# Kernel tuning notes

Measured on AMD Instinct MI355X. Metric: run time of the kernel, lower is better.

Reference implementation:

```python
import jax, jax.numpy as jnp
import numpy as np

INPUT_DIM, HIDDEN, OUT_DIM = 7, 64, 4


def _lstm_layer(x_seq, W_ih, W_hh, b_ih, b_hh):
    """Single LSTM layer, batch_first x_seq [B,T,D] -> [B,T,H]. PyTorch gate order i,f,g,o."""
    B = x_seq.shape[0]
    H = W_hh.shape[1]
    # Precompute input projection for all timesteps (hoist GEMM out of the scan).
    x_proj = jnp.einsum('btd,gd->btg', x_seq, W_ih) + b_ih + b_hh  # [B,T,4H]

    def step(carry, xt):
        h, c = carry
        gates = xt + h @ W_hh.T  # [B,4H]
        i, f, g, o = jnp.split(gates, 4, axis=-1)
        i = jax.nn.sigmoid(i)
        f = jax.nn.sigmoid(f)
        g = jnp.tanh(g)
        o = jax.nn.sigmoid(o)
        c = f * c + i * g
        h = o * jnp.tanh(c)
        return (h, c), h

    h0 = jnp.zeros((B, H), x_seq.dtype)
    c0 = jnp.zeros((B, H), x_seq.dtype)
    (_, _), hs = jax.lax.scan(step, (h0, c0), jnp.swapaxes(x_proj, 0, 1))  # hs [T,B,H]
    return jnp.swapaxes(hs, 0, 1)  # [B,T,H]


def setup_inputs() -> dict:
    key = jax.random.key(0)
    ks = jax.random.split(key, 12)
    s = 0.1  # init scale ~ 1/sqrt(hidden)
    x = jax.random.normal(ks[0], (4096, 512, INPUT_DIM), dtype=jnp.float32)
    W_ih0 = jax.random.normal(ks[1], (4 * HIDDEN, INPUT_DIM), dtype=jnp.float32) * s
    W_hh0 = jax.random.normal(ks[2], (4 * HIDDEN, HIDDEN), dtype=jnp.float32) * s
    b_ih0 = jax.random.normal(ks[3], (4 * HIDDEN,), dtype=jnp.float32) * s
    b_hh0 = jax.random.normal(ks[4], (4 * HIDDEN,), dtype=jnp.float32) * s
    W_ih1 = jax.random.normal(ks[5], (4 * HIDDEN, HIDDEN), dtype=jnp.float32) * s
    W_hh1 = jax.random.normal(ks[6], (4 * HIDDEN, HIDDEN), dtype=jnp.float32) * s
    b_ih1 = jax.random.normal(ks[7], (4 * HIDDEN,), dtype=jnp.float32) * s
    b_hh1 = jax.random.normal(ks[8], (4 * HIDDEN,), dtype=jnp.float32) * s
    W_fc = jax.random.normal(ks[9], (OUT_DIM, HIDDEN), dtype=jnp.float32) * s
    b_fc = jax.random.normal(ks[10], (OUT_DIM,), dtype=jnp.float32) * s
    return {"x": x, "W_ih0": W_ih0, "W_hh0": W_hh0, "b_ih0": b_ih0, "b_hh0": b_hh0,
            "W_ih1": W_ih1, "W_hh1": W_hh1, "b_ih1": b_ih1, "b_hh1": b_hh1,
            "W_fc": W_fc, "b_fc": b_fc}


def reference(x, W_ih0, W_hh0, b_ih0, b_hh0, W_ih1, W_hh1, b_ih1, b_hh1, W_fc, b_fc):
    h1 = _lstm_layer(x, W_ih0, W_hh0, b_ih0, b_hh0)   # [B,T,H]
    h2 = _lstm_layer(h1, W_ih1, W_hh1, b_ih1, b_hh1)  # [B,T,H]
    last = h2[:, -1, :]                               # [B,H]
    return last @ W_fc.T + b_fc                       # [B,4]
```

## Files before the change

kernel.cpp:

```cpp
#include <hip/hip_runtime.h>

#define T_SEQ 512
#define HID 64
#define MB 16
#define NTHREADS 1024
#define A1STR 104
#define A2STR 72

typedef __attribute__((ext_vector_type(8))) short short8;
typedef __attribute__((ext_vector_type(4))) float floatx4;

#define LOG2E 1.4426950408889634f

__device__ __forceinline__ float bf2f(short b) {
  return __uint_as_float(((unsigned)(unsigned short)b) << 16);
}
__device__ __forceinline__ short f2bf_rne(float v) {
  unsigned u = __float_as_uint(v);
  return (short)((u + 0x7FFFu + ((u >> 16) & 1u)) >> 16);
}
__device__ __forceinline__ float rcp_(float x) { return __builtin_amdgcn_rcpf(x); }
__device__ __forceinline__ float sigm_p(float ap) {
  return rcp_(1.f + __builtin_amdgcn_exp2f(-ap));
}
__device__ __forceinline__ float tanh_p(float yp) {
  return 1.f - 2.f * rcp_(__builtin_amdgcn_exp2f(yp) + 1.f);
}
__device__ __forceinline__ float tanh_c(float c) {
  return tanh_p((2.f * LOG2E) * c);
}

__device__ __forceinline__ short w1elem(int k, int n, float wsc,
                                        const float* __restrict__ Wih0,
                                        const float* __restrict__ Whh0) {
  float v;
  if      (k < 64) { v = Whh0[n*64 + k]; }
  else if (k < 71) { v = Wih0[n*7 + (k - 64)]; }
  else return (short)0;
  return f2bf_rne(v * wsc);
}
__device__ __forceinline__ short w2elem(int k, int n, float wsc,
                                        const float* __restrict__ Wih1,
                                        const float* __restrict__ Whh1) {
  float v;
  if (k < 64) { v = Wih1[n*64 + k]; }
  else        { v = Whh1[n*64 + (k - 64)]; }
  return f2bf_rne(v * wsc);
}

#define MFMA(A, B, C) __builtin_amdgcn_mfma_f32_16x16x32_bf16((A), (B), (C), 0, 0, 0)

__global__ __launch_bounds__(NTHREADS, 4) void lstm_fused(
    const float* __restrict__ x,
    const float* __restrict__ Wih0, const float* __restrict__ Whh0,
    const float* __restrict__ bih0, const float* __restrict__ bhh0,
    const float* __restrict__ Wih1, const float* __restrict__ Whh1,
    const float* __restrict__ bih1, const float* __restrict__ bhh1,
    const float* __restrict__ Wfc,  const float* __restrict__ bfc,
    float* __restrict__ out)
{
  __shared__ __align__(16) short A1[2][MB][A1STR];
  __shared__ __align__(16) short A2[2][MB][A2STR];
  __shared__ float h2f[MB][HID + 4];

  const int tid  = threadIdx.x;
  const int lane = tid & 63;
  const int wave = tid >> 6;
  const int l15  = lane & 15;
  const int quad = lane >> 4;
  const int quad8= quad * 8;
  const int g4   = l15 & 3;
  const int b0   = blockIdx.x * MB;
  const int un   = wave * 4 + quad;
  const int n    = g4 * 64 + (wave * 4 + (l15 >> 2));
  const float wsc = (g4 == 2) ? 2.f * LOG2E : LOG2E;

  for (int i = tid; i < 2*MB*A1STR/2; i += NTHREADS) ((unsigned*)A1)[i] = 0u;
  for (int i = tid; i < 2*MB*A2STR/2; i += NTHREADS) ((unsigned*)A2)[i] = 0u;

  floatx4 bi1v, bi2v;
  #pragma unroll
  for (int g = 0; g < 4; ++g) {
    float ws = (g == 2) ? 2.f * LOG2E : LOG2E;
    bi1v[g] = (bih0[g*64 + un] + bhh0[g*64 + un]) * ws;
    bi2v[g] = (bih1[g*64 + un] + bhh1[g*64 + un]) * ws;
  }

  const int xb = tid / 7, xd = tid - xb * 7;
  const float* xbase = x + ((size_t)(b0 + (xb & 15)) * T_SEQ) * 7 + xd;
  float xcur = 0.f;
  if (tid < 112) {
    A1[0][xb][64 + xd] = f2bf_rne(xbase[0]);
    xcur = xbase[7];
  }

  short8 B1f[3];
  short8 B2f[4];
  #pragma unroll
  for (int ks = 0; ks < 3; ++ks) {
    short8 f;
    #pragma unroll
    for (int jj = 0; jj < 8; ++jj) f[jj] = w1elem(ks*32 + quad8 + jj, n, wsc, Wih0, Whh0);
    B1f[ks] = f;
  }
  #pragma unroll
  for (int ks = 0; ks < 4; ++ks) {
    short8 f;
    #pragma unroll
    for (int jj = 0; jj < 8; ++jj) f[jj] = w2elem(ks*32 + quad8 + jj, n, wsc, Wih1, Whh1);
    B2f[ks] = f;
  }
  __syncthreads();

  float c1 = 0.f, c2 = 0.f;

#define STEP_X(NXT, XT)                                                      \
    if (tid < 112) {                                                         \
      A1[NXT][xb][64 + xd] = f2bf_rne(xcur);                                 \
      xcur = xbase[7 * (XT)];                                                \
    }

#define STEP_FULL(CUR, NXT, IT)                                              \
  {                                                                          \
    int xt_ = (IT) + 2; if (xt_ > T_SEQ - 1) xt_ = T_SEQ - 1;                \
    STEP_X(NXT, xt_)                                                         \
    short8 hf0 = *(const short8*)&A1[CUR][l15][      quad8];                 \
    short8 hf1 = *(const short8*)&A1[CUR][l15][ 32 + quad8];                 \
    short8 hfx = *(const short8*)&A1[CUR][l15][ 64 + quad8];                 \
    short8 h20 = *(const short8*)&A2[CUR][l15][      quad8];                 \
    short8 h21 = *(const short8*)&A2[CUR][l15][ 32 + quad8];                 \
    floatx4 p1 = bi1v;                                                       \
    p1 = MFMA(B1f[0], hf0, p1);                                              \
    p1 = MFMA(B1f[1], hf1, p1);                                              \
    p1 = MFMA(B1f[2], hfx, p1);                                              \
    floatx4 p2 = bi2v;                                                       \
    p2 = MFMA(B2f[0], hf0, p2);                                              \
    p2 = MFMA(B2f[1], hf1, p2);                                              \
    p2 = MFMA(B2f[2], h20, p2);                                              \
    p2 = MFMA(B2f[3], h21, p2);                                              \
    {                                                                        \
      float iv = sigm_p(p1[0]), fv = sigm_p(p1[1]);                          \
      float gv = tanh_p(p1[2]), ov = sigm_p(p1[3]);                          \
      c1 = fv * c1 + iv * gv;                                                \
      A1[NXT][l15][un] = f2bf_rne(ov * tanh_c(c1));                          \
    }                                                                        \
    {                                                                        \
      float iv = sigm_p(p2[0]), fv = sigm_p(p2[1]);                          \
      float gv = tanh_p(p2[2]), ov = sigm_p(p2[3]);                          \
      c2 = fv * c2 + iv * gv;                                                \
      A2[NXT][l15][un] = f2bf_rne(ov * tanh_c(c2));                          \
    }                                                                        \
    __syncthreads();                                                         \
  }

  {
    STEP_X(1, 2)
    short8 hf0 = *(const short8*)&A1[0][l15][      quad8];
    short8 hf1 = *(const short8*)&A1[0][l15][ 32 + quad8];
    short8 hfx = *(const short8*)&A1[0][l15][ 64 + quad8];
    floatx4 p1 = bi1v;
    p1 = MFMA(B1f[0], hf0, p1);
    p1 = MFMA(B1f[1], hf1, p1);
    p1 = MFMA(B1f[2], hfx, p1);
    float iv = sigm_p(p1[0]), fv = sigm_p(p1[1]);
    float gv = tanh_p(p1[2]), ov = sigm_p(p1[3]);
    c1 = fv * c1 + iv * gv;
    A1[1][l15][un] = f2bf_rne(ov * tanh_c(c1));
    __syncthreads();
  }

  #pragma unroll 1
  for (int k = 0; k < 255; ++k) {
    STEP_FULL(1, 0, 2*k + 1)
    STEP_FULL(0, 1, 2*k + 2)
  }
  STEP_FULL(1, 0, 511)

  {
    short8 hf0 = *(const short8*)&A1[0][l15][      quad8];
    short8 hf1 = *(const short8*)&A1[0][l15][ 32 + quad8];
    short8 h20 = *(const short8*)&A2[0][l15][      quad8];
    short8 h21 = *(const short8*)&A2[0][l15][ 32 + quad8];
    floatx4 p2 = bi2v;
    p2 = MFMA(B2f[0], hf0, p2);
    p2 = MFMA(B2f[1], hf1, p2);
    p2 = MFMA(B2f[2], h20, p2);
    p2 = MFMA(B2f[3], h21, p2);
    float iv = sigm_p(p2[0]), fv = sigm_p(p2[1]);
    float gv = tanh_p(p2[2]), ov = sigm_p(p2[3]);
    c2 = fv * c2 + iv * gv;
    h2f[l15][un] = ov * tanh_c(c2);
    __syncthreads();
  }

  if (tid < MB * 4) {
    int bbf = tid >> 2, o = tid & 3;
    float acc = bfc[o];
    #pragma unroll 8
    for (int kk = 0; kk < HID; ++kk) acc += h2f[bbf][kk] * Wfc[o*HID + kk];
    out[(size_t)(b0 + bbf) * 4 + o] = acc;
  }
}

extern "C" void kernel_launch(void* const* d_in, const int* in_sizes, int n_in,
                              void* d_out, int out_size, void* d_ws, size_t ws_size,
                              hipStream_t stream) {
  const float* x    = (const float*)d_in[0];
  const float* Wih0 = (const float*)d_in[1];
  const float* Whh0 = (const float*)d_in[2];
  const float* bih0 = (const float*)d_in[3];
  const float* bhh0 = (const float*)d_in[4];
  const float* Wih1 = (const float*)d_in[5];
  const float* Whh1 = (const float*)d_in[6];
  const float* bih1 = (const float*)d_in[7];
  const float* bhh1 = (const float*)d_in[8];
  const float* Wfc  = (const float*)d_in[9];
  const float* bfc  = (const float*)d_in[10];
  (void)d_ws; (void)ws_size; (void)n_in; (void)out_size;

  const int B = in_sizes[0] / (T_SEQ * 7);
  dim3 grid(B / MB);
  lstm_fused<<<grid, NTHREADS, 0, stream>>>(x, Wih0, Whh0, bih0, bhh0,
                                            Wih1, Whh1, bih1, bhh1, Wfc, bfc,
                                            (float*)d_out);
}
```

Baseline: 471.5 us.

## Specialize waves per LSTM layer with two units per lane and packed stores

Splits the 16 waves so waves 0-7 compute only layer 1 and waves 8-15 compute only layer 2. Each lane now handles two hidden units, giving two independent MFMA chains per wave. Weight columns are permuted so each lane's two outputs land next to each other, which allows a single packed 32-bit bf16 store to LDS. The aim is to remove the per-wave serial dependency between the layer-1 and layer-2 MFMA chains and gain instruction-level parallelism. The cost is uneven work between the two wave groups (layer 2 has four K-steps versus three) and more live registers per lane.

```diff
diff --git a/kernel.cpp b/kernel.cpp
--- a/kernel.cpp
+++ b/kernel.cpp
@@ -12,9 +12,6 @@
 
 #define LOG2E 1.4426950408889634f
 
-__device__ __forceinline__ float bf2f(short b) {
-  return __uint_as_float(((unsigned)(unsigned short)b) << 16);
-}
 __device__ __forceinline__ short f2bf_rne(float v) {
   unsigned u = __float_as_uint(v);
   return (short)((u + 0x7FFFu + ((u >> 16) & 1u)) >> 16);
@@ -28,13 +25,17 @@
 }
 __device__ __forceinline__ float tanh_c(float c) {
   return tanh_p((2.f * LOG2E) * c);
+}
+
+__device__ __forceinline__ int uofp(int p) {
+  return (p & ~7) + ((p & 7) >> 1) + ((p & 1) << 2);
 }
 
 __device__ __forceinline__ short w1elem(int k, int n, float wsc,
                                         const float* __restrict__ Wih0,
                                         const float* __restrict__ Whh0) {
   float v;
-  if      (k < 64) { v = Whh0[n*64 + k]; }
+  if      (k < 64) { v = Whh0[n*64 + uofp(k)]; }
   else if (k < 71) { v = Wih0[n*7 + (k - 64)]; }
   else return (short)0;
   return f2bf_rne(v * wsc);
@@ -43,12 +44,16 @@
                                         const float* __restrict__ Wih1,
                                         const float* __restrict__ Whh1) {
   float v;
-  if (k < 64) { v = Wih1[n*64 + k]; }
-  else        { v = Whh1[n*64 + (k - 64)]; }
+  if (k < 64) { v = Wih1[n*64 + uofp(k)]; }
+  else        { v = Whh1[n*64 + uofp(k - 64)]; }
   return f2bf_rne(v * wsc);
 }
 
 #define MFMA(A, B, C) __builtin_amdgcn_mfma_f32_16x16x32_bf16((A), (B), (C), 0, 0, 0)
+
+#define PACK2(ha, hb)                                                        \
+  ((unsigned)(unsigned short)f2bf_rne(ha) |                                  \
+   ((unsigned)(unsigned short)f2bf_rne(hb) << 16))
 
 __global__ __launch_bounds__(NTHREADS, 4) void lstm_fused(
     const float* __restrict__ x,
@@ -66,106 +71,131 @@
   const int tid  = threadIdx.x;
   const int lane = tid & 63;
   const int wave = tid >> 6;
+  const int wl   = wave & 7;
+  const bool isL1 = wave < 8;
   const int l15  = lane & 15;
   const int quad = lane >> 4;
   const int quad8= quad * 8;
   const int g4   = l15 & 3;
   const int b0   = blockIdx.x * MB;
-  const int un   = wave * 4 + quad;
-  const int n    = g4 * 64 + (wave * 4 + (l15 >> 2));
+  const int u0   = wl*8 + quad;
+  const int u1   = u0 + 4;
+  const int hpos = wl*8 + 2*quad;
+  const int n0   = g4*64 + (wl*8 + (l15 >> 2));
+  const int n1   = n0 + 4;
   const float wsc = (g4 == 2) ? 2.f * LOG2E : LOG2E;
 
   for (int i = tid; i < 2*MB*A1STR/2; i += NTHREADS) ((unsigned*)A1)[i] = 0u;
   for (int i = tid; i < 2*MB*A2STR/2; i += NTHREADS) ((unsigned*)A2)[i] = 0u;
 
-  floatx4 bi1v, bi2v;
+  const float* bi_ = isL1 ? bih0 : bih1;
+  const float* bh_ = isL1 ? bhh0 : bhh1;
+  floatx4 bia, bib;
   #pragma unroll
   for (int g = 0; g < 4; ++g) {
     float ws = (g == 2) ? 2.f * LOG2E : LOG2E;
-    bi1v[g] = (bih0[g*64 + un] + bhh0[g*64 + un]) * ws;
-    bi2v[g] = (bih1[g*64 + un] + bhh1[g*64 + un]) * ws;
-  }
-
-  const int xb = tid / 7, xd = tid - xb * 7;
-  const float* xbase = x + ((size_t)(b0 + (xb & 15)) * T_SEQ) * 7 + xd;
+    bia[g] = (bi_[g*64 + u0] + bh_[g*64 + u0]) * ws;
+    bib[g] = (bi_[g*64 + u1] + bh_[g*64 + u1]) * ws;
+  }
+
+  const int xd   = lane & 31;
+  const int xrow = 2*wl + (lane >> 5);
+  const bool xact = isL1 && (xd < 7);
+  const float* xbase = x + ((size_t)(b0 + xrow) * T_SEQ) * 7 + xd;
   float xcur = 0.f;
-  if (tid < 112) {
-    A1[0][xb][64 + xd] = f2bf_rne(xbase[0]);
+  if (xact) {
+    A1[0][xrow][64 + xd] = f2bf_rne(xbase[0]);
     xcur = xbase[7];
   }
 
-  short8 B1f[3];
-  short8 B2f[4];
-  #pragma unroll
-  for (int ks = 0; ks < 3; ++ks) {
-    short8 f;
+  short8 WA[4], WB[4];
+  if (isL1) {
     #pragma unroll
-    for (int jj = 0; jj < 8; ++jj) f[jj] = w1elem(ks*32 + quad8 + jj, n, wsc, Wih0, Whh0);
-    B1f[ks] = f;
-  }
-  #pragma unroll
-  for (int ks = 0; ks < 4; ++ks) {
-    short8 f;
+    for (int ks = 0; ks < 3; ++ks) {
+      short8 fa, fb;
+      #pragma unroll
+      for (int jj = 0; jj < 8; ++jj) {
+        fa[jj] = w1elem(ks*32 + quad8 + jj, n0, wsc, Wih0, Whh0);
+        fb[jj] = w1elem(ks*32 + quad8 + jj, n1, wsc, Wih0, Whh0);
+      }
+      WA[ks] = fa; WB[ks] = fb;
+    }
+  } else {
     #pragma unroll
-    for (int jj = 0; jj < 8; ++jj) f[jj] = w2elem(ks*32 + quad8 + jj, n, wsc, Wih1, Whh1);
-    B2f[ks] = f;
+    for (int ks = 0; ks < 4; ++ks) {
+      short8 fa, fb;
+      #pragma unroll
+      for (int jj = 0; jj < 8; ++jj) {
+        fa[jj] = w2elem(ks*32 + quad8 + jj, n0, wsc, Wih1, Whh1);
+        fb[jj] = w2elem(ks*32 + quad8 + jj, n1, wsc, Wih1, Whh1);
+      }
+      WA[ks] = fa; WB[ks] = fb;
+    }
   }
   __syncthreads();
 
-  float c1 = 0.f, c2 = 0.f;
+  float ca = 0.f, cb = 0.f;
 
 #define STEP_X(NXT, XT)                                                      \
-    if (tid < 112) {                                                         \
-      A1[NXT][xb][64 + xd] = f2bf_rne(xcur);                                 \
+    if (xact) {                                                              \
+      A1[NXT][xrow][64 + xd] = f2bf_rne(xcur);                               \
       xcur = xbase[7 * (XT)];                                                \
     }
+
+#define EW2(PA, PB, HA, HB)                                                  \
+    { float iv = sigm_p(PA[0]), fv = sigm_p(PA[1]);                          \
+      float gv = tanh_p(PA[2]), ov = sigm_p(PA[3]);                          \
+      ca = fv * ca + iv * gv;  HA = ov * tanh_c(ca); }                       \
+    { float iv = sigm_p(PB[0]), fv = sigm_p(PB[1]);                          \
+      float gv = tanh_p(PB[2]), ov = sigm_p(PB[3]);                          \
+      cb = fv * cb + iv * gv;  HB = ov * tanh_c(cb); }
 
 #define STEP_FULL(CUR, NXT, IT)                                              \
   {                                                                          \
-    int xt_ = (IT) + 2; if (xt_ > T_SEQ - 1) xt_ = T_SEQ - 1;                \
-    STEP_X(NXT, xt_)                                                         \
-    short8 hf0 = *(const short8*)&A1[CUR][l15][      quad8];                 \
-    short8 hf1 = *(const short8*)&A1[CUR][l15][ 32 + quad8];                 \
-    short8 hfx = *(const short8*)&A1[CUR][l15][ 64 + quad8];                 \
-    short8 h20 = *(const short8*)&A2[CUR][l15][      quad8];                 \
-    short8 h21 = *(const short8*)&A2[CUR][l15][ 32 + quad8];                 \
-    floatx4 p1 = bi1v;                                                       \
-    p1 = MFMA(B1f[0], hf0, p1);                                              \
-    p1 = MFMA(B1f[1], hf1, p1);                                              \
-    p1 = MFMA(B1f[2], hfx, p1);                                              \
-    floatx4 p2 = bi2v;                                                       \
-    p2 = MFMA(B2f[0], hf0, p2);                                              \
-    p2 = MFMA(B2f[1], hf1, p2);                                              \
-    p2 = MFMA(B2f[2], h20, p2);                                              \
-    p2 = MFMA(B2f[3], h21, p2);                                              \
-    {                                                                        \
-      float iv = sigm_p(p1[0]), fv = sigm_p(p1[1]);                          \
-      float gv = tanh_p(p1[2]), ov = sigm_p(p1[3]);                          \
-      c1 = fv * c1 + iv * gv;                                                \
-      A1[NXT][l15][un] = f2bf_rne(ov * tanh_c(c1));                          \
-    }                                                                        \
-    {                                                                        \
-      float iv = sigm_p(p2[0]), fv = sigm_p(p2[1]);                          \
-      float gv = tanh_p(p2[2]), ov = sigm_p(p2[3]);                          \
-      c2 = fv * c2 + iv * gv;                                                \
-      A2[NXT][l15][un] = f2bf_rne(ov * tanh_c(c2));                          \
+    if (isL1) {                                                              \
+      int xt_ = (IT) + 2; if (xt_ > T_SEQ - 1) xt_ = T_SEQ - 1;              \
+      STEP_X(NXT, xt_)                                                       \
+      short8 hf0 = *(const short8*)&A1[CUR][l15][     quad8];                \
+      short8 hf1 = *(const short8*)&A1[CUR][l15][32 + quad8];                \
+      short8 hfx = *(const short8*)&A1[CUR][l15][64 + quad8];                \
+      floatx4 pa = bia, pb = bib;                                            \
+      pa = MFMA(WA[0], hf0, pa);  pb = MFMA(WB[0], hf0, pb);                 \
+      pa = MFMA(WA[1], hf1, pa);  pb = MFMA(WB[1], hf1, pb);                 \
+      pa = MFMA(WA[2], hfx, pa);  pb = MFMA(WB[2], hfx, pb);                 \
+      float ha, hb;                                                          \
+      EW2(pa, pb, ha, hb)                                                    \
+      *(unsigned*)&A1[NXT][l15][hpos] = PACK2(ha, hb);                       \
+    } else {                                                                 \
+      short8 hf0 = *(const short8*)&A1[CUR][l15][     quad8];                \
+      short8 hf1 = *(const short8*)&A1[CUR][l15][32 + quad8];                \
+      short8 h20 = *(const short8*)&A2[CUR][l15][     quad8];                \
+      short8 h21 = *(const short8*)&A2[CUR][l15][32 + quad8];                \
+      floatx4 pa = bia, pb = bib;                                            \
+      pa = MFMA(WA[0], hf0, pa);  pb = MFMA(WB[0], hf0, pb);                 \
+      pa = MFMA(WA[1], hf1, pa);  pb = MFMA(WB[1], hf1, pb);                 \
+      pa = MFMA(WA[2], h20, pa);  pb = MFMA(WB[2], h20, pb);                 \
+      pa = MFMA(WA[3], h21, pa);  pb = MFMA(WB[3], h21, pb);                 \
+      float ha, hb;                                                          \
+      EW2(pa, pb, ha, hb)                                                    \
+      *(unsigned*)&A2[NXT][l15][hpos] = PACK2(ha, hb);                       \
     }                                                                        \
     __syncthreads();                                                         \
   }
 
   {
-    STEP_X(1, 2)
-    short8 hf0 = *(const short8*)&A1[0][l15][      quad8];
-    short8 hf1 = *(const short8*)&A1[0][l15][ 32 + quad8];
-    short8 hfx = *(const short8*)&A1[0][l15][ 64 + quad8];
-    floatx4 p1 = bi1v;
-    p1 = MFMA(B1f[0], hf0, p1);
-    p1 = MFMA(B1f[1], hf1, p1);
-    p1 = MFMA(B1f[2], hfx, p1);
-    float iv = sigm_p(p1[0]), fv = sigm_p(p1[1]);
-    float gv = tanh_p(p1[2]), ov = sigm_p(p1[3]);
-    c1 = fv * c1 + iv * gv;
-    A1[1][l15][un] = f2bf_rne(ov * tanh_c(c1));
+    if (isL1) {
+      STEP_X(1, 2)
+      short8 hf0 = *(const short8*)&A1[0][l15][     quad8];
+      short8 hf1 = *(const short8*)&A1[0][l15][32 + quad8];
+      short8 hfx = *(const short8*)&A1[0][l15][64 + quad8];
+      floatx4 pa = bia, pb = bib;
+      pa = MFMA(WA[0], hf0, pa);  pb = MFMA(WB[0], hf0, pb);
+      pa = MFMA(WA[1], hf1, pa);  pb = MFMA(WB[1], hf1, pb);
+      pa = MFMA(WA[2], hfx, pa);  pb = MFMA(WB[2], hfx, pb);
+      float ha, hb;
+      EW2(pa, pb, ha, hb)
+      *(unsigned*)&A1[1][l15][hpos] = PACK2(ha, hb);
+    }
     __syncthreads();
   }
 
@@ -177,19 +207,21 @@
   STEP_FULL(1, 0, 511)
 
   {
-    short8 hf0 = *(const short8*)&A1[0][l15][      quad8];
-    short8 hf1 = *(const short8*)&A1[0][l15][ 32 + quad8];
-    short8 h20 = *(const short8*)&A2[0][l15][      quad8];
-    short8 h21 = *(const short8*)&A2[0][l15][ 32 + quad8];
-    floatx4 p2 = bi2v;
-    p2 = MFMA(B2f[0], hf0, p2);
-    p2 = MFMA(B2f[1], hf1, p2);
-    p2 = MFMA(B2f[2], h20, p2);
-    p2 = MFMA(B2f[3], h21, p2);
-    float iv = sigm_p(p2[0]), fv = sigm_p(p2[1]);
-    float gv = tanh_p(p2[2]), ov = sigm_p(p2[3]);
-    c2 = fv * c2 + iv * gv;
-    h2f[l15][un] = ov * tanh_c(c2);
+    if (!isL1) {
+      short8 hf0 = *(const short8*)&A1[0][l15][     quad8];
+      short8 hf1 = *(const short8*)&A1[0][l15][32 + quad8];
+      short8 h20 = *(const short8*)&A2[0][l15][     quad8];
+      short8 h21 = *(const short8*)&A2[0][l15][32 + quad8];
+      floatx4 pa = bia, pb = bib;
+      pa = MFMA(WA[0], hf0, pa);  pb = MFMA(WB[0], hf0, pb);
+      pa = MFMA(WA[1], hf1, pa);  pb = MFMA(WB[1], hf1, pb);
+      pa = MFMA(WA[2], h20, pa);  pb = MFMA(WB[2], h20, pb);
+      pa = MFMA(WA[3], h21, pa);  pb = MFMA(WB[3], h21, pb);
+      float ha, hb;
+      EW2(pa, pb, ha, hb)
+      h2f[l15][u0] = ha;
+      h2f[l15][u1] = hb;
+    }
     __syncthreads();
   }
 
```

After: 447.3 us. 1.05x faster.
